# Performance work log

Hardware: AMD Instinct MI355X
Metric: run time of the kernel (lower is better)

Reference implementation:

```python
import jax, jax.numpy as jnp
import numpy as np
from jax import lax

T, B, E, H, L = 256, 128, 512, 1024, 2


def setup_inputs() -> dict:
    key = jax.random.key(0)
    ks = jax.random.split(key, 12)
    x = jax.random.normal(ks[0], (T, B, E), dtype=jnp.float32)
    # PackedSequence batch_sizes: descending, first == max batch
    bs = jnp.sort(jax.random.randint(ks[1], (T,), 1, B + 1).astype(jnp.int32))[::-1]
    bs = bs.at[0].set(B)
    unsorted_indices = jax.random.permutation(ks[2], B).astype(jnp.int32)
    s = 1.0 / np.sqrt(H)
    def u(k, shape):
        return jax.random.uniform(k, shape, jnp.float32, -s, s)
    return {
        "x": x,
        "W_ih0": u(ks[3], (3 * H, E)), "W_hh0": u(ks[4], (3 * H, H)),
        "b_ih0": u(ks[5], (3 * H,)), "b_hh0": u(ks[6], (3 * H,)),
        "W_ih1": u(ks[7], (3 * H, H)), "W_hh1": u(ks[8], (3 * H, H)),
        "b_ih1": u(ks[9], (3 * H,)), "b_hh1": u(ks[10], (3 * H,)),
        "batch_sizes": bs,
        "unsorted_indices": unsorted_indices,
    }


def gru_cell(x, h, W_ih, W_hh, b_ih, b_hh):
    gi = x @ W_ih.T + b_ih          # [b, 3H]
    gh = h @ W_hh.T + b_hh          # [b, 3H]
    i_r, i_z, i_n = jnp.split(gi, 3, axis=-1)
    h_r, h_z, h_n = jnp.split(gh, 3, axis=-1)
    r = jax.nn.sigmoid(i_r + h_r)
    z = jax.nn.sigmoid(i_z + h_z)
    n = jnp.tanh(i_n + r * h_n)
    return (1.0 - z) * n + z * h


def reference(x, W_ih0, W_hh0, b_ih0, b_hh0, W_ih1, W_hh1, b_ih1, b_hh1,
              batch_sizes, unsorted_indices):
    params = [(W_ih0, W_hh0, b_ih0, b_hh0), (W_ih1, W_hh1, b_ih1, b_hh1)]
    row = jnp.arange(B)

    def step(h, inp):
        xt, bs = inp                       # xt: [B, E]
        mask = (row < bs)[:, None]         # active rows this timestep
        layer_in = xt
        new_h = []
        for i in range(L):
            hn = gru_cell(layer_in, h[i], *params[i])
            # inactive rows keep their previous hidden state (packed-seq semantics)
            new_h.append(jnp.where(mask, hn, h[i]))
            layer_in = hn
        return jnp.stack(new_h), None

    h0 = jnp.zeros((L, B, H), dtype=x.dtype)
    h_final, _ = lax.scan(step, h0, (x, batch_sizes))
    # index_select(h, 1, unsorted_indices)
    return h_final[:, unsorted_indices, :]
```

## Files before the change

kernel.cpp:

```cpp
#include <hip/hip_runtime.h>
#include <cstdint>
#include <cstddef>

#define T_ 256
#define B_ 128
#define E_ 512
#define H_ 1024
#define BH (B_*H_)
#define GI (B_*3072)
#define GATHER_BID 64

typedef _Float16 v8h __attribute__((ext_vector_type(8)));
typedef float    v4f __attribute__((ext_vector_type(4)));
typedef unsigned int u32x4 __attribute__((ext_vector_type(4)));

__device__ __forceinline__ float sigmoidf_(float x) {
    return 1.0f / (1.0f + __expf(-x));
}
__device__ __forceinline__ float tanhf_(float x) {
    return 1.0f - 2.0f / (__expf(2.0f * x) + 1.0f);
}

__device__ __forceinline__ void sc_store2(void* p, unsigned v) {
    asm volatile("global_store_short %0, %1, off sc0 sc1" :: "v"(p), "v"(v) : "memory");
}
__device__ __forceinline__ void sc_store4(void* p, float v) {
    asm volatile("global_store_dword %0, %1, off sc0 sc1" :: "v"(p), "v"(v) : "memory");
}

#define LBAR() do { \
    asm volatile("s_waitcnt lgkmcnt(0)" ::: "memory"); \
    __builtin_amdgcn_s_barrier(); \
    asm volatile("" ::: "memory"); \
} while (0)

__global__ __launch_bounds__(256, 1) void gru_persist(
    const int* __restrict__ bs,
    const _Float16* __restrict__ x16,
    const _Float16* __restrict__ Wi0,
    const _Float16* __restrict__ Wh0,
    const _Float16* __restrict__ Wi1,
    const _Float16* __restrict__ Wh1,
    const float* __restrict__ bias,
    float* __restrict__ h0f, float* __restrict__ h1f,
    _Float16* __restrict__ h0h, _Float16* __restrict__ h1h,
    _Float16* __restrict__ hn0,
    float* __restrict__ gi0,
    int* __restrict__ flags,
    int* __restrict__ epoch)
{
    __shared__ _Float16 WL[55296];
    __shared__ _Float16 AS[2][128][72];

    const int bid = blockIdx.x;
    const int tid = threadIdx.x;
    const int lane = tid & 63, w = tid >> 6;
    const int m = lane & 15, q = lane >> 4;
    const int srow = tid >> 1, spart = tid & 1;
    const int stage = (bid < 64) ? 0 : (bid < 128) ? 1 : 2;
    const int sl = (stage == 0) ? bid : (stage == 1) ? bid - 64 : bid - 128;

    if (stage == 0) {
        for (int u = tid; u < 8 * 384; u += 256) {
            int kc = u / 384, rem = u % 384, c = rem >> 3, slot = rem & 7;
            int gr = sl * 48 + c;
            *(u32x4*)&WL[(kc * 48 + c) * 72 + slot * 8] =
                *(const u32x4*)(Wi0 + (size_t)gr * E_ + kc * 64 + slot * 8);
        }
    } else if (stage == 1) {
        for (int u = tid; u < 16 * 384; u += 256) {
            int kc = u / 384, rem = u % 384, c = rem >> 3, slot = rem & 7;
            int gr = (c >> 4) * 1024 + sl * 16 + (c & 15);
            *(u32x4*)&WL[(kc * 48 + c) * 72 + slot * 8] =
                *(const u32x4*)(Wh0 + (size_t)gr * H_ + kc * 64 + slot * 8);
        }
    } else {
        for (int u = tid; u < 32 * 192; u += 256) {
            int kc = u / 192, rem = u % 192, c = rem >> 3, slot = rem & 7;
            int gr = (c >> 3) * 1024 + sl * 8 + (c & 7);
            const _Float16* src = (kc < 16) ? (Wi1 + (size_t)gr * H_ + kc * 64)
                                            : (Wh1 + (size_t)gr * H_ + (kc - 16) * 64);
            *(u32x4*)&WL[(kc * 24 + c) * 72 + slot * 8] = *(const u32x4*)(src + slot * 8);
        }
    }
    __syncthreads();

    float br = 0.f, bz = 0.f, bi = 0.f, bh = 0.f;
    int colE = 0;
    if (stage == 1) {
        colE = sl * 16 + m;
        br = bias[colE]; bz = bias[H_ + colE];
        bi = bias[2 * H_ + colE]; bh = bias[3 * H_ + colE];
    } else if (stage == 2) {
        colE = sl * 8 + (m & 7);
        const float* bb = bias + 4 * H_;
        br = bb[colE]; bz = bb[H_ + colE];
        bi = bb[2 * H_ + colE]; bh = bb[3 * H_ + colE];
    }
    float hm[2][4];
#pragma unroll
    for (int rf = 0; rf < 2; ++rf)
#pragma unroll
        for (int r = 0; r < 4; ++r) hm[rf][r] = 0.f;

    v4f acc[6];
    u32x4 QA0, QA1, QA2, QA3, QB0, QB1, QB2, QB3;
    u32x4 QC0, QC1, QC2, QC3, QD0, QD1, QD2, QD3;

#define ISSUE(Qv, kcn) do { \
        const _Float16* p_ = sp + (size_t)(kcn) * 64; \
        Qv##0 = *(const u32x4*)(p_ + 0);  Qv##1 = *(const u32x4*)(p_ + 8); \
        Qv##2 = *(const u32x4*)(p_ + 16); Qv##3 = *(const u32x4*)(p_ + 24); \
    } while (0)
#define WRITEQ(Qv, dbuf) do { \
        _Float16* d_ = &AS[dbuf][srow][spart * 32]; \
        *(u32x4*)(d_ + 0) = Qv##0;  *(u32x4*)(d_ + 8)  = Qv##1; \
        *(u32x4*)(d_ + 16) = Qv##2; *(u32x4*)(d_ + 24) = Qv##3; \
    } while (0)
#define COMPUTE3(BUF, KC) do { \
        const _Float16* wch_ = &WL[(KC) * 48 * 72]; \
        _Pragma("unroll") \
        for (int s = 0; s < 2; ++s) { \
            const int ko = s * 32 + q * 8; \
            v8h a0 = *(const v8h*)&AS[BUF][32 * w + m][ko]; \
            v8h a1 = *(const v8h*)&AS[BUF][32 * w + 16 + m][ko]; \
            _Pragma("unroll") \
            for (int g = 0; g < 3; ++g) { \
                v8h b = *(const v8h*)&wch_[(g * 16 + m) * 72 + ko]; \
                acc[g * 2 + 0] = __builtin_amdgcn_mfma_f32_16x16x32_f16(a0, b, acc[g * 2 + 0], 0, 0, 0); \
                acc[g * 2 + 1] = __builtin_amdgcn_mfma_f32_16x16x32_f16(a1, b, acc[g * 2 + 1], 0, 0, 0); \
            } \
        } \
    } while (0)
#define CHUNK3(KC, QI, QW, BUF) do { \
        if ((KC) + 4 < nch) ISSUE(QI, (KC) + 4); \
        COMPUTE3(BUF, KC); \
        if ((KC) + 1 < nch) WRITEQ(QW, (BUF) ^ 1); \
        LBAR(); \
    } while (0)
#define COMPUTE2(BUF, KC, ANB) do { \
        const _Float16* wch_ = &WL[(KC) * 24 * 72]; \
        _Pragma("unroll") \
        for (int s = 0; s < 2; ++s) { \
            const int ko = s * 32 + q * 8; \
            v8h a0 = *(const v8h*)&AS[BUF][32 * w + m][ko]; \
            v8h a1 = *(const v8h*)&AS[BUF][32 * w + 16 + m][ko]; \
            v8h b0 = *(const v8h*)&wch_[(m) * 72 + ko]; \
            v8h b1 = *(const v8h*)&wch_[(8 + m) * 72 + ko]; \
            acc[0] = __builtin_amdgcn_mfma_f32_16x16x32_f16(a0, b0, acc[0], 0, 0, 0); \
            acc[1] = __builtin_amdgcn_mfma_f32_16x16x32_f16(a1, b0, acc[1], 0, 0, 0); \
            acc[(ANB) + 0] = __builtin_amdgcn_mfma_f32_16x16x32_f16(a0, b1, acc[(ANB) + 0], 0, 0, 0); \
            acc[(ANB) + 1] = __builtin_amdgcn_mfma_f32_16x16x32_f16(a1, b1, acc[(ANB) + 1], 0, 0, 0); \
        } \
    } while (0)
#define SUBLOOP2(KB, ANB) do { \
        ISSUE(QA, 0); ISSUE(QB, 1); ISSUE(QC, 2); ISSUE(QD, 3); \
        WRITEQ(QA, 0); \
        LBAR(); \
        for (int base = 0; base < 16; base += 4) { \
            if (base + 4 < 16) ISSUE(QA, base + 4); \
            COMPUTE2(0, (KB) + base + 0, ANB); \
            if (base + 1 < 16) WRITEQ(QB, 1); \
            LBAR(); \
            if (base + 5 < 16) ISSUE(QB, base + 5); \
            COMPUTE2(1, (KB) + base + 1, ANB); \
            if (base + 2 < 16) WRITEQ(QC, 0); \
            LBAR(); \
            if (base + 6 < 16) ISSUE(QC, base + 6); \
            COMPUTE2(0, (KB) + base + 2, ANB); \
            if (base + 3 < 16) WRITEQ(QD, 1); \
            LBAR(); \
            if (base + 7 < 16) ISSUE(QD, base + 7); \
            COMPUTE2(1, (KB) + base + 3, ANB); \
            if (base + 4 < 16) WRITEQ(QA, 0); \
            LBAR(); \
        } \
    } while (0)

#define WAIT_EPOCH(KV, DO_INV) do { \
        if (tid == 0) { \
            while (__hip_atomic_load(epoch, __ATOMIC_RELAXED, __HIP_MEMORY_SCOPE_AGENT) < (KV)) \
                __builtin_amdgcn_s_sleep(1); \
            if (DO_INV) (void)__hip_atomic_load(epoch, __ATOMIC_ACQUIRE, __HIP_MEMORY_SCOPE_AGENT); \
        } \
        __syncthreads(); \
    } while (0)
#define DO_BARRIER(KV) do { \
        __syncthreads(); \
        if (tid == 0) \
            __hip_atomic_store(&flags[bid], (KV) + 1, __ATOMIC_RELEASE, __HIP_MEMORY_SCOPE_AGENT); \
        if (bid == GATHER_BID && tid < 64) { \
            const int tgt = (KV) + 1; \
            for (;;) { \
                int f0 = __hip_atomic_load(&flags[tid],       __ATOMIC_RELAXED, __HIP_MEMORY_SCOPE_AGENT); \
                int f1 = __hip_atomic_load(&flags[tid + 64],  __ATOMIC_RELAXED, __HIP_MEMORY_SCOPE_AGENT); \
                int f2 = __hip_atomic_load(&flags[tid + 128], __ATOMIC_RELAXED, __HIP_MEMORY_SCOPE_AGENT); \
                int f3 = __hip_atomic_load(&flags[tid + 192], __ATOMIC_RELAXED, __HIP_MEMORY_SCOPE_AGENT); \
                bool ok = (f0 >= tgt) && (f1 >= tgt) && (f2 >= tgt) && (f3 >= tgt); \
                if (__all(ok)) break; \
                __builtin_amdgcn_s_sleep(1); \
            } \
            if (tid == 0) \
                __hip_atomic_store(epoch, (KV) + 1, __ATOMIC_RELEASE, __HIP_MEMORY_SCOPE_AGENT); \
        } \
    } while (0)

    for (int k = 0; k < T_ + 2; ++k) {
        if (stage == 0) {
            const bool active = (k < T_);
            if (active) {
                const int t = k;
#pragma unroll
                for (int i = 0; i < 6; ++i) acc[i] = (v4f){0.f, 0.f, 0.f, 0.f};
                const _Float16* sp = x16 + (size_t)t * B_ * E_ + (size_t)srow * E_ + spart * 32;
                const int nch = 8;
                ISSUE(QA, 0); ISSUE(QB, 1); ISSUE(QC, 2); ISSUE(QD, 3);
                WRITEQ(QA, 0);
                LBAR();
                CHUNK3(0, QA, QB, 0); CHUNK3(1, QB, QC, 1);
                CHUNK3(2, QC, QD, 0); CHUNK3(3, QD, QA, 1);
                CHUNK3(4, QA, QB, 0); CHUNK3(5, QB, QC, 1);
                CHUNK3(6, QC, QD, 0); CHUNK3(7, QD, QA, 1);
                WAIT_EPOCH(k, false);
                float* gw = gi0 + (size_t)(t & 1) * GI;
                const int cbase = sl * 48;
#pragma unroll
                for (int cf = 0; cf < 3; ++cf)
#pragma unroll
                    for (int rf = 0; rf < 2; ++rf)
#pragma unroll
                        for (int r = 0; r < 4; ++r) {
                            int row = 32 * w + rf * 16 + q * 4 + r;
                            sc_store4(gw + (size_t)row * 3072 + cbase + cf * 16 + m,
                                      acc[cf * 2 + rf][r]);
                        }
            }
        } else if (stage == 1) {
            const bool active = (k >= 1) && (k <= T_);
            if (active) {
                const int t = k - 1;
                WAIT_EPOCH(k, true);
                const int bs_t = bs[t];
                const int pb = t & 1, rb = pb ^ 1;
#pragma unroll
                for (int i = 0; i < 6; ++i) acc[i] = (v4f){0.f, 0.f, 0.f, 0.f};
                const _Float16* sp = h0h + (size_t)rb * BH + (size_t)srow * H_ + spart * 32;
                const int nch = 16;
                ISSUE(QA, 0); ISSUE(QB, 1); ISSUE(QC, 2); ISSUE(QD, 3);
                WRITEQ(QA, 0);
                LBAR();
                for (int base = 0; base < 16; base += 4) {
                    CHUNK3(base + 0, QA, QB, 0); CHUNK3(base + 1, QB, QC, 1);
                    CHUNK3(base + 2, QC, QD, 0); CHUNK3(base + 3, QD, QA, 1);
                }
                const float* gr_ = gi0 + (size_t)pb * GI;
                _Float16* hh_w = h0h + (size_t)pb * BH;
                _Float16* hn0w = hn0 + (size_t)pb * BH;
#pragma unroll
                for (int rf = 0; rf < 2; ++rf)
#pragma unroll
                    for (int r = 0; r < 4; ++r) {
                        int row = 32 * w + rf * 16 + q * 4 + r;
                        size_t go = (size_t)row * 3072 + colE;
                        float gir = gr_[go];
                        float giz = gr_[go + 1024];
                        float gin = gr_[go + 2048];
                        size_t off = (size_t)row * H_ + colE;
                        float hprev = hm[rf][r];
                        float rr = sigmoidf_(gir + acc[0 + rf][r] + br);
                        float zz = sigmoidf_(giz + acc[2 + rf][r] + bz);
                        float nn = tanhf_(gin + bi + rr * (acc[4 + rf][r] + bh));
                        float hnew = (1.0f - zz) * nn + zz * hprev;
                        bool act = row < bs_t;
                        float hsel = act ? hnew : hprev;
                        sc_store2(hn0w + off, (unsigned)__builtin_bit_cast(unsigned short, (_Float16)hnew));
                        sc_store2(hh_w + off, (unsigned)__builtin_bit_cast(unsigned short, (_Float16)hsel));
                        hm[rf][r] = hsel;
                    }
            } else if (bid == GATHER_BID) {
                WAIT_EPOCH(k, false);
            }
        } else {
            const bool active = (k >= 2);
            if (active) {
                const int t = k - 2;
                WAIT_EPOCH(k, true);
                const int bs_t = bs[t];
                const int pb = t & 1, rb = pb ^ 1;
#pragma unroll
                for (int i = 0; i < 6; ++i) acc[i] = (v4f){0.f, 0.f, 0.f, 0.f};
                {
                    const _Float16* sp = hn0 + (size_t)pb * BH + (size_t)srow * H_ + spart * 32;
                    SUBLOOP2(0, 2);
                }
                {
                    const _Float16* sp = h1h + (size_t)rb * BH + (size_t)srow * H_ + spart * 32;
                    SUBLOOP2(16, 4);
                }
                _Float16* hh_w = h1h + (size_t)pb * BH;
#pragma unroll
                for (int rf = 0; rf < 2; ++rf)
#pragma unroll
                    for (int r = 0; r < 4; ++r) {
                        int row = 32 * w + rf * 16 + q * 4 + r;
                        float zz_s = __shfl_xor(acc[0 + rf][r], 8);
                        float inx  = __shfl_xor(acc[2 + rf][r], 8);
                        float hnh  = __shfl_xor(acc[4 + rf][r], 8);
                        float hprev = hm[rf][r];
                        float rr = sigmoidf_(acc[0 + rf][r] + br);
                        float zz = sigmoidf_(zz_s + bz);
                        float nn = tanhf_(inx + bi + rr * (hnh + bh));
                        float hnew = (1.0f - zz) * nn + zz * hprev;
                        bool act = row < bs_t;
                        float hsel = act ? hnew : hprev;
                        if (m < 8) {
                            size_t off = (size_t)row * H_ + colE;
                            sc_store2(hh_w + off, (unsigned)__builtin_bit_cast(unsigned short, (_Float16)hsel));
                        }
                        hm[rf][r] = hsel;
                    }
            }
        }

        if (k < T_ + 1) DO_BARRIER(k);
    }

    if (stage == 1) {
#pragma unroll
        for (int rf = 0; rf < 2; ++rf)
#pragma unroll
            for (int r = 0; r < 4; ++r) {
                int row = 32 * w + rf * 16 + q * 4 + r;
                h0f[(size_t)row * H_ + colE] = hm[rf][r];
            }
    } else if (stage == 2 && m < 8) {
#pragma unroll
        for (int rf = 0; rf < 2; ++rf)
#pragma unroll
            for (int r = 0; r < 4; ++r) {
                int row = 32 * w + rf * 16 + q * 4 + r;
                h1f[(size_t)row * H_ + colE] = hm[rf][r];
            }
    }
}

__global__ void cvt_f32_f16(const float* __restrict__ s, _Float16* __restrict__ d, int n) {
    int i = (blockIdx.x * 256 + threadIdx.x) * 8;
    if (i >= n) return;
    float4 v0 = *(const float4*)(s + i);
    float4 v1 = *(const float4*)(s + i + 4);
    v8h o = { (_Float16)v0.x, (_Float16)v0.y, (_Float16)v0.z, (_Float16)v0.w,
              (_Float16)v1.x, (_Float16)v1.y, (_Float16)v1.z, (_Float16)v1.w };
    *(v8h*)(d + i) = o;
}

__global__ void prep_bias(const float* __restrict__ bi0, const float* __restrict__ bh0,
                          const float* __restrict__ bi1, const float* __restrict__ bh1,
                          float* __restrict__ bias) {
    int tid = blockIdx.x * 256 + threadIdx.x;
    int l = tid >> 10, j = tid & 1023;
    const float* bi = l ? bi1 : bi0;
    const float* bh = l ? bh1 : bh0;
    float* o = bias + l * 4 * H_;
    o[j]           = bi[j] + bh[j];
    o[H_ + j]      = bi[H_ + j] + bh[H_ + j];
    o[2 * H_ + j]  = bi[2 * H_ + j];
    o[3 * H_ + j]  = bh[2 * H_ + j];
}

__global__ void gather_out(const float* __restrict__ h0f, const float* __restrict__ h1f,
                           const int* __restrict__ unsorted, float* __restrict__ out) {
    int rowid = blockIdx.x;
    int l = rowid >> 7, b = rowid & 127;
    int src = unsorted[b];
    const float* s = (l ? h1f : h0f) + (size_t)src * H_;
    float* o = out + (size_t)rowid * H_;
    int c = threadIdx.x * 4;
    *(float4*)(o + c) = *(const float4*)(s + c);
}

extern "C" void kernel_launch(void* const* d_in, const int* in_sizes, int n_in,
                              void* d_out, int out_size, void* d_ws, size_t ws_size,
                              hipStream_t stream) {
    const float* x    = (const float*)d_in[0];
    const float* Wi0f = (const float*)d_in[1];
    const float* Wh0f = (const float*)d_in[2];
    const float* bi0  = (const float*)d_in[3];
    const float* bh0  = (const float*)d_in[4];
    const float* Wi1f = (const float*)d_in[5];
    const float* Wh1f = (const float*)d_in[6];
    const float* bi1  = (const float*)d_in[7];
    const float* bh1  = (const float*)d_in[8];
    const int*  bs       = (const int*)d_in[9];
    const int*  unsorted = (const int*)d_in[10];
    float* out = (float*)d_out;

    char* ws = (char*)d_ws;
    size_t off = 0;
    auto alloc = [&](size_t bytes) -> char* {
        char* p = ws + off;
        off += (bytes + 255) & ~(size_t)255;
        return p;
    };
    _Float16* x16 = (_Float16*)alloc((size_t)T_ * B_ * E_ * 2);
    _Float16* Wi0 = (_Float16*)alloc((size_t)3 * H_ * E_ * 2);
    _Float16* Wh0 = (_Float16*)alloc((size_t)3 * H_ * H_ * 2);
    _Float16* Wi1 = (_Float16*)alloc((size_t)3 * H_ * H_ * 2);
    _Float16* Wh1 = (_Float16*)alloc((size_t)3 * H_ * H_ * 2);
    float*    bias = (float*)alloc(2 * 4 * H_ * 4);
    float*    gi0  = (float*)alloc((size_t)2 * GI * 4);
    float*    h0f  = (float*)alloc((size_t)BH * 4);
    float*    h1f  = (float*)alloc((size_t)BH * 4);
    char* zbase = ws + off;
    _Float16* h0h = (_Float16*)alloc((size_t)2 * BH * 2);
    _Float16* h1h = (_Float16*)alloc((size_t)2 * BH * 2);
    _Float16* hn0 = (_Float16*)alloc((size_t)2 * BH * 2);
    int*      flags = (int*)alloc(1024);
    int*      epoch = (int*)alloc(256);
    size_t zbytes = (size_t)((ws + off) - zbase);

    (void)hipMemsetAsync(zbase, 0, zbytes, stream);

    cvt_f32_f16<<<(T_ * B_ * E_) / 2048, 256, 0, stream>>>(x, x16, T_ * B_ * E_);
    cvt_f32_f16<<<(3 * H_ * E_) / 2048, 256, 0, stream>>>(Wi0f, Wi0, 3 * H_ * E_);
    cvt_f32_f16<<<(3 * H_ * H_) / 2048, 256, 0, stream>>>(Wh0f, Wh0, 3 * H_ * H_);
    cvt_f32_f16<<<(3 * H_ * H_) / 2048, 256, 0, stream>>>(Wi1f, Wi1, 3 * H_ * H_);
    cvt_f32_f16<<<(3 * H_ * H_) / 2048, 256, 0, stream>>>(Wh1f, Wh1, 3 * H_ * H_);
    prep_bias<<<8, 256, 0, stream>>>(bi0, bh0, bi1, bh1, bias);

    gru_persist<<<256, 256, 0, stream>>>(bs, x16, Wi0, Wh0, Wi1, Wh1, bias,
                                         h0f, h1f, h0h, h1h, hn0, gi0, flags, epoch);
    gather_out<<<256, 256, 0, stream>>>(h0f, h1f, unsorted, out);
}
```

Measured before the change: 4.925 ms.

## Use cache-bypassing loads and relaxed atomics in persistent GRU pipeline barrier

Loads of cross-block data (x16, hn0, h0h/h1h, gi0) now go through inline-asm global loads with sc0 sc1 cache bypass and explicit vmcnt waits. That allows the acquire invalidation in the epoch wait and the release semantics on flag and epoch stores to be replaced by relaxed atomics. The chunk pipelines are fully unrolled with explicit drain phases, and the gi0 gate loads are batched ahead of the epilogue. This aims to cut cache-invalidate and fence cost at every timestep barrier. The risk is memory-ordering correctness, since it relies on the sc stores and loads being coherent without fences.

```diff
diff --git a/kernel.cpp b/kernel.cpp
--- a/kernel.cpp
+++ b/kernel.cpp
@@ -27,7 +27,20 @@
 __device__ __forceinline__ void sc_store4(void* p, float v) {
     asm volatile("global_store_dword %0, %1, off sc0 sc1" :: "v"(p), "v"(v) : "memory");
 }
-
+__device__ __forceinline__ u32x4 sc_load16_q(const void* p) {
+    u32x4 v;
+    asm volatile("global_load_dwordx4 %0, %1, off sc0 sc1" : "=v"(v) : "v"(p));
+    return v;
+}
+__device__ __forceinline__ float sc_load4f(const void* p) {
+    float v;
+    asm volatile("global_load_dword %0, %1, off sc0 sc1" : "=v"(v) : "v"(p));
+    return v;
+}
+#define VW(N) do { \
+    asm volatile("s_waitcnt vmcnt(" #N ")" ::: "memory"); \
+    __builtin_amdgcn_sched_barrier(0); \
+} while (0)
 #define LBAR() do { \
     asm volatile("s_waitcnt lgkmcnt(0)" ::: "memory"); \
     __builtin_amdgcn_s_barrier(); \
@@ -107,10 +120,10 @@
     u32x4 QA0, QA1, QA2, QA3, QB0, QB1, QB2, QB3;
     u32x4 QC0, QC1, QC2, QC3, QD0, QD1, QD2, QD3;
 
-#define ISSUE(Qv, kcn) do { \
+#define SCLOAD(Qv, kcn) do { \
         const _Float16* p_ = sp + (size_t)(kcn) * 64; \
-        Qv##0 = *(const u32x4*)(p_ + 0);  Qv##1 = *(const u32x4*)(p_ + 8); \
-        Qv##2 = *(const u32x4*)(p_ + 16); Qv##3 = *(const u32x4*)(p_ + 24); \
+        Qv##0 = sc_load16_q(p_ + 0);  Qv##1 = sc_load16_q(p_ + 8); \
+        Qv##2 = sc_load16_q(p_ + 16); Qv##3 = sc_load16_q(p_ + 24); \
     } while (0)
 #define WRITEQ(Qv, dbuf) do { \
         _Float16* d_ = &AS[dbuf][srow][spart * 32]; \
@@ -132,12 +145,6 @@
             } \
         } \
     } while (0)
-#define CHUNK3(KC, QI, QW, BUF) do { \
-        if ((KC) + 4 < nch) ISSUE(QI, (KC) + 4); \
-        COMPUTE3(BUF, KC); \
-        if ((KC) + 1 < nch) WRITEQ(QW, (BUF) ^ 1); \
-        LBAR(); \
-    } while (0)
 #define COMPUTE2(BUF, KC, ANB) do { \
         const _Float16* wch_ = &WL[(KC) * 24 * 72]; \
         _Pragma("unroll") \
@@ -153,42 +160,51 @@
             acc[(ANB) + 1] = __builtin_amdgcn_mfma_f32_16x16x32_f16(a1, b1, acc[(ANB) + 1], 0, 0, 0); \
         } \
     } while (0)
-#define SUBLOOP2(KB, ANB) do { \
-        ISSUE(QA, 0); ISSUE(QB, 1); ISSUE(QC, 2); ISSUE(QD, 3); \
-        WRITEQ(QA, 0); \
-        LBAR(); \
-        for (int base = 0; base < 16; base += 4) { \
-            if (base + 4 < 16) ISSUE(QA, base + 4); \
-            COMPUTE2(0, (KB) + base + 0, ANB); \
-            if (base + 1 < 16) WRITEQ(QB, 1); \
-            LBAR(); \
-            if (base + 5 < 16) ISSUE(QB, base + 5); \
-            COMPUTE2(1, (KB) + base + 1, ANB); \
-            if (base + 2 < 16) WRITEQ(QC, 0); \
-            LBAR(); \
-            if (base + 6 < 16) ISSUE(QC, base + 6); \
-            COMPUTE2(0, (KB) + base + 2, ANB); \
-            if (base + 3 < 16) WRITEQ(QD, 1); \
-            LBAR(); \
-            if (base + 7 < 16) ISSUE(QD, base + 7); \
-            COMPUTE2(1, (KB) + base + 3, ANB); \
-            if (base + 4 < 16) WRITEQ(QA, 0); \
-            LBAR(); \
-        } \
-    } while (0)
-
-#define WAIT_EPOCH(KV, DO_INV) do { \
+#define PRO() do { \
+        SCLOAD(QA, 0); SCLOAD(QB, 1); SCLOAD(QC, 2); SCLOAD(QD, 3); \
+        VW(12); WRITEQ(QA, 0); LBAR(); \
+    } while (0)
+#define CH3(J, QF, QW) do { \
+        SCLOAD(QF, (J) + 4); \
+        COMPUTE3((J) & 1, J); \
+        VW(12); WRITEQ(QW, ((J) + 1) & 1); LBAR(); \
+    } while (0)
+#define DRAIN3(NCH) do { \
+        COMPUTE3(0, (NCH) - 4); VW(8); WRITEQ(QB, 1); LBAR(); \
+        COMPUTE3(1, (NCH) - 3); VW(4); WRITEQ(QC, 0); LBAR(); \
+        COMPUTE3(0, (NCH) - 2); VW(0); WRITEQ(QD, 1); LBAR(); \
+        COMPUTE3(1, (NCH) - 1); LBAR(); \
+    } while (0)
+#define CH2(J, QF, QW, KB, ANB) do { \
+        SCLOAD(QF, (J) + 4); \
+        COMPUTE2((J) & 1, (KB) + (J), ANB); \
+        VW(12); WRITEQ(QW, ((J) + 1) & 1); LBAR(); \
+    } while (0)
+#define SUBGEMM2(KB, ANB) do { \
+        PRO(); \
+        CH2(0, QA, QB, KB, ANB); CH2(1, QB, QC, KB, ANB); \
+        CH2(2, QC, QD, KB, ANB); CH2(3, QD, QA, KB, ANB); \
+        CH2(4, QA, QB, KB, ANB); CH2(5, QB, QC, KB, ANB); \
+        CH2(6, QC, QD, KB, ANB); CH2(7, QD, QA, KB, ANB); \
+        CH2(8, QA, QB, KB, ANB); CH2(9, QB, QC, KB, ANB); \
+        CH2(10, QC, QD, KB, ANB); CH2(11, QD, QA, KB, ANB); \
+        COMPUTE2(0, (KB) + 12, ANB); VW(8); WRITEQ(QB, 1); LBAR(); \
+        COMPUTE2(1, (KB) + 13, ANB); VW(4); WRITEQ(QC, 0); LBAR(); \
+        COMPUTE2(0, (KB) + 14, ANB); VW(0); WRITEQ(QD, 1); LBAR(); \
+        COMPUTE2(1, (KB) + 15, ANB); LBAR(); \
+    } while (0)
+
+#define WAIT_EPOCH(KV) do { \
         if (tid == 0) { \
             while (__hip_atomic_load(epoch, __ATOMIC_RELAXED, __HIP_MEMORY_SCOPE_AGENT) < (KV)) \
                 __builtin_amdgcn_s_sleep(1); \
-            if (DO_INV) (void)__hip_atomic_load(epoch, __ATOMIC_ACQUIRE, __HIP_MEMORY_SCOPE_AGENT); \
         } \
         __syncthreads(); \
     } while (0)
 #define DO_BARRIER(KV) do { \
         __syncthreads(); \
         if (tid == 0) \
-            __hip_atomic_store(&flags[bid], (KV) + 1, __ATOMIC_RELEASE, __HIP_MEMORY_SCOPE_AGENT); \
+            __hip_atomic_store(&flags[bid], (KV) + 1, __ATOMIC_RELAXED, __HIP_MEMORY_SCOPE_AGENT); \
         if (bid == GATHER_BID && tid < 64) { \
             const int tgt = (KV) + 1; \
             for (;;) { \
@@ -201,27 +217,21 @@
                 __builtin_amdgcn_s_sleep(1); \
             } \
             if (tid == 0) \
-                __hip_atomic_store(epoch, (KV) + 1, __ATOMIC_RELEASE, __HIP_MEMORY_SCOPE_AGENT); \
+                __hip_atomic_store(epoch, (KV) + 1, __ATOMIC_RELAXED, __HIP_MEMORY_SCOPE_AGENT); \
         } \
     } while (0)
 
     for (int k = 0; k < T_ + 2; ++k) {
         if (stage == 0) {
-            const bool active = (k < T_);
-            if (active) {
+            if (k < T_) {
                 const int t = k;
 #pragma unroll
                 for (int i = 0; i < 6; ++i) acc[i] = (v4f){0.f, 0.f, 0.f, 0.f};
                 const _Float16* sp = x16 + (size_t)t * B_ * E_ + (size_t)srow * E_ + spart * 32;
-                const int nch = 8;
-                ISSUE(QA, 0); ISSUE(QB, 1); ISSUE(QC, 2); ISSUE(QD, 3);
-                WRITEQ(QA, 0);
-                LBAR();
-                CHUNK3(0, QA, QB, 0); CHUNK3(1, QB, QC, 1);
-                CHUNK3(2, QC, QD, 0); CHUNK3(3, QD, QA, 1);
-                CHUNK3(4, QA, QB, 0); CHUNK3(5, QB, QC, 1);
-                CHUNK3(6, QC, QD, 0); CHUNK3(7, QD, QA, 1);
-                WAIT_EPOCH(k, false);
+                PRO();
+                CH3(0, QA, QB); CH3(1, QB, QC); CH3(2, QC, QD); CH3(3, QD, QA);
+                DRAIN3(8);
+                WAIT_EPOCH(k);
                 float* gw = gi0 + (size_t)(t & 1) * GI;
                 const int cbase = sl * 48;
 #pragma unroll
@@ -236,24 +246,32 @@
                         }
             }
         } else if (stage == 1) {
-            const bool active = (k >= 1) && (k <= T_);
-            if (active) {
+            if (k >= 1 && k <= T_) {
                 const int t = k - 1;
-                WAIT_EPOCH(k, true);
+                WAIT_EPOCH(k);
                 const int bs_t = bs[t];
                 const int pb = t & 1, rb = pb ^ 1;
 #pragma unroll
                 for (int i = 0; i < 6; ++i) acc[i] = (v4f){0.f, 0.f, 0.f, 0.f};
                 const _Float16* sp = h0h + (size_t)rb * BH + (size_t)srow * H_ + spart * 32;
-                const int nch = 16;
-                ISSUE(QA, 0); ISSUE(QB, 1); ISSUE(QC, 2); ISSUE(QD, 3);
-                WRITEQ(QA, 0);
-                LBAR();
-                for (int base = 0; base < 16; base += 4) {
-                    CHUNK3(base + 0, QA, QB, 0); CHUNK3(base + 1, QB, QC, 1);
-                    CHUNK3(base + 2, QC, QD, 0); CHUNK3(base + 3, QD, QA, 1);
-                }
+                PRO();
+                CH3(0, QA, QB); CH3(1, QB, QC); CH3(2, QC, QD); CH3(3, QD, QA);
+                CH3(4, QA, QB); CH3(5, QB, QC); CH3(6, QC, QD); CH3(7, QD, QA);
+                CH3(8, QA, QB); CH3(9, QB, QC); CH3(10, QC, QD); CH3(11, QD, QA);
+                DRAIN3(16);
                 const float* gr_ = gi0 + (size_t)pb * GI;
+                float gv[2][4][3];
+#pragma unroll
+                for (int rf = 0; rf < 2; ++rf)
+#pragma unroll
+                    for (int r = 0; r < 4; ++r) {
+                        int row = 32 * w + rf * 16 + q * 4 + r;
+                        const float* gp = gr_ + (size_t)row * 3072 + colE;
+#pragma unroll
+                        for (int g = 0; g < 3; ++g)
+                            gv[rf][r][g] = sc_load4f(gp + g * 1024);
+                    }
+                VW(0);
                 _Float16* hh_w = h0h + (size_t)pb * BH;
                 _Float16* hn0w = hn0 + (size_t)pb * BH;
 #pragma unroll
@@ -261,15 +279,11 @@
 #pragma unroll
                     for (int r = 0; r < 4; ++r) {
                         int row = 32 * w + rf * 16 + q * 4 + r;
-                        size_t go = (size_t)row * 3072 + colE;
-                        float gir = gr_[go];
-                        float giz = gr_[go + 1024];
-                        float gin = gr_[go + 2048];
                         size_t off = (size_t)row * H_ + colE;
                         float hprev = hm[rf][r];
-                        float rr = sigmoidf_(gir + acc[0 + rf][r] + br);
-                        float zz = sigmoidf_(giz + acc[2 + rf][r] + bz);
-                        float nn = tanhf_(gin + bi + rr * (acc[4 + rf][r] + bh));
+                        float rr = sigmoidf_(gv[rf][r][0] + acc[0 + rf][r] + br);
+                        float zz = sigmoidf_(gv[rf][r][1] + acc[2 + rf][r] + bz);
+                        float nn = tanhf_(gv[rf][r][2] + bi + rr * (acc[4 + rf][r] + bh));
                         float hnew = (1.0f - zz) * nn + zz * hprev;
                         bool act = row < bs_t;
                         float hsel = act ? hnew : hprev;
@@ -278,24 +292,23 @@
                         hm[rf][r] = hsel;
                     }
             } else if (bid == GATHER_BID) {
-                WAIT_EPOCH(k, false);
+                WAIT_EPOCH(k);
             }
         } else {
-            const bool active = (k >= 2);
-            if (active) {
+            if (k >= 2) {
                 const int t = k - 2;
-                WAIT_EPOCH(k, true);
+                WAIT_EPOCH(k);
                 const int bs_t = bs[t];
                 const int pb = t & 1, rb = pb ^ 1;
 #pragma unroll
                 for (int i = 0; i < 6; ++i) acc[i] = (v4f){0.f, 0.f, 0.f, 0.f};
                 {
                     const _Float16* sp = hn0 + (size_t)pb * BH + (size_t)srow * H_ + spart * 32;
-                    SUBLOOP2(0, 2);
+                    SUBGEMM2(0, 2);
                 }
                 {
                     const _Float16* sp = h1h + (size_t)rb * BH + (size_t)srow * H_ + spart * 32;
-                    SUBLOOP2(16, 4);
+                    SUBGEMM2(16, 4);
                 }
                 _Float16* hh_w = h1h + (size_t)pb * BH;
 #pragma unroll
@@ -333,7 +346,7 @@
                 int row = 32 * w + rf * 16 + q * 4 + r;
                 h0f[(size_t)row * H_ + colE] = hm[rf][r];
             }
-    } else if (stage == 2 && m < 8) {
+    } else if (stage == 2 && (m & 15) < 8) {
 #pragma unroll
         for (int rf = 0; rf < 2; ++rf)
 #pragma unroll
```

New measurement: 4.972 ms. No clear change (+0.9%).
